# Kernel optimization log

Hardware: AMD Instinct MI355X
Metric: run time of the kernel (lower is better)

Reference implementation:

```python
import jax, jax.numpy as jnp
import numpy as np

N = 25000   # num nodes
E = 500000  # num edges
B = 4       # num queries (batch)
D = 32      # hidden dim
R2 = 474    # doubled num_relation
L = 4       # num conv layers
EPS = 1e-6


def setup_inputs() -> dict:
    key = jax.random.key(0)
    ks = jax.random.split(key, 12)
    return {
        "node_in": jax.random.randint(ks[0], (E,), 0, N),
        "node_out": jax.random.randint(ks[1], (E,), 0, N),
        "relation": jax.random.randint(ks[2], (E,), 0, R2),
        "edge_weight": jnp.ones((E,), jnp.float32),
        "h_index": jax.random.randint(ks[3], (B,), 0, N),
        "r_index": jax.random.randint(ks[4], (B,), 0, R2),
        "query_embed": jax.random.normal(ks[5], (R2, D), jnp.float32) * 0.1,
        "rel_W": jax.random.normal(ks[6], (L, D, R2 * D), jnp.float32) * 0.05,
        "rel_b": jnp.zeros((L, R2 * D), jnp.float32),
        "lin_W": jax.random.normal(ks[7], (L, 13 * D, D), jnp.float32) * 0.05,
        "lin_b": jnp.zeros((L, D), jnp.float32),
        "mlp_W1": jax.random.normal(ks[8], (2 * D, 2 * D), jnp.float32) * 0.05,
        "mlp_b1": jnp.zeros((2 * D,), jnp.float32),
        "mlp_W2": jax.random.normal(ks[9], (2 * D, 1), jnp.float32) * 0.05,
        "mlp_b2": jnp.zeros((1,), jnp.float32),
    }


def _nbfnet(node_in, node_out, relation, h_index, r_index,
            edge_weight, query_embed, rel_W, rel_b, lin_W, lin_b,
            mlp_W1, mlp_b1, mlp_W2, mlp_b2):
    query = query_embed[r_index]                                   # [B, D]
    # boundary condition: query embedding placed at the head node of each query
    boundary = jnp.zeros((N, B, D), query.dtype).at[h_index, jnp.arange(B)].set(query)
    # append one self-entry per node (boundary message), as in the torch code
    node_out_ext = jnp.concatenate([node_out, jnp.arange(N)])      # [E+N]
    w_ext = jnp.concatenate([edge_weight, jnp.ones((N,), edge_weight.dtype)])[:, None, None]
    cnt = jax.ops.segment_sum(jnp.ones((E + N,), query.dtype), node_out_ext, N)[:, None, None]
    deg = jax.ops.segment_sum(edge_weight, node_out, N) + 1.0      # degree_out + 1, [N]
    scale = jnp.log(deg)
    scale = scale / scale.mean()
    scales = jnp.stack([jnp.ones_like(scale), scale, 1.0 / jnp.clip(scale, 0.01)], -1)  # [N,3]

    hidden = boundary
    for l in range(L):
        # dependent relation embeddings: [R2, B, D]
        rel_in = (query @ rel_W[l] + rel_b[l]).reshape(B, R2, D).transpose(1, 0, 2)
        # distmult message + boundary self-message: [E+N, B, D]
        msg = jnp.concatenate([rel_in[relation] * hidden[node_in], boundary], 0)
        mw = msg * w_ext
        mean = jax.ops.segment_sum(mw, node_out_ext, N) / cnt
        sq_mean = jax.ops.segment_sum(msg * mw, node_out_ext, N) / cnt
        mx = jax.ops.segment_max(mw, node_out_ext, N)
        mn = jax.ops.segment_min(mw, node_out_ext, N)
        std = jnp.sqrt(jnp.clip(sq_mean - mean * mean, EPS))
        feat = jnp.stack([mean, mx, mn, std], -1).reshape(N, B, 4 * D)   # PNA stats
        update = (feat[..., None] * scales[:, None, None, :]).reshape(N, B, 12 * D)
        hidden = jax.nn.relu(jnp.concatenate([hidden, update], -1) @ lin_W[l] + lin_b[l])

    feat = jnp.concatenate([hidden, jnp.broadcast_to(query[None], (N, B, D))], -1)  # [N,B,2D]
    h1 = jax.nn.relu(feat @ mlp_W1 + mlp_b1)
    score = (h1 @ mlp_W2 + mlp_b2)[..., 0]                          # [N, B]
    return score.T                                                  # [B, N]


def reference(node_in, node_out, relation, edge_weight, h_index, r_index,
              query_embed, rel_W, rel_b, lin_W, lin_b,
              mlp_W1, mlp_b1, mlp_W2, mlp_b2):
    return _nbfnet(node_in, node_out, relation, h_index, r_index,
                   edge_weight, query_embed, rel_W, rel_b, lin_W, lin_b,
                   mlp_W1, mlp_b1, mlp_W2, mlp_b2)
```

## Files before the change

kernel.cpp:

```cpp
#include <hip/hip_runtime.h>
#include <hip/hip_fp16.h>

#define NN  25000
#define EE  500000
#define BB  4
#define DD  32
#define LL  4
#define R2C 474
#define BD  128
#define THD 416
#define EPSF 1e-6f
#define WMH 13312

typedef _Float16 half8 __attribute__((ext_vector_type(8)));
typedef _Float16 h2v   __attribute__((ext_vector_type(2)));
typedef float    f32x4 __attribute__((ext_vector_type(4)));
typedef float    f2v   __attribute__((ext_vector_type(2)));

__global__ __launch_bounds__(256) void pidx_kernel(const int4* __restrict__ no4,
                                                   int* __restrict__ cnt,
                                                   int4* __restrict__ pidx4) {
  int i = blockIdx.x * 256 + threadIdx.x;
  if (i >= EE / 4) return;
  int4 d = no4[i];
  int4 r;
  r.x = atomicAdd(&cnt[d.x], 1);
  r.y = atomicAdd(&cnt[d.y], 1);
  r.z = atomicAdd(&cnt[d.z], 1);
  r.w = atomicAdd(&cnt[d.w], 1);
  pidx4[i] = r;
}

__global__ __launch_bounds__(256) void prep_kernel(const int* __restrict__ cnt,
                                                   int* __restrict__ base,
                                                   int* __restrict__ gcnt) {
  int n = blockIdx.x * 256 + threadIdx.x;
  if (n >= NN) return;
  base[n] = atomicAdd(gcnt, (cnt[n] + 1) & ~1);
}

__global__ __launch_bounds__(256) void scatter_kernel(const int4* __restrict__ ni4,
                                                      const int4* __restrict__ no4,
                                                      const int4* __restrict__ rl4,
                                                      const float4* __restrict__ ew4,
                                                      const int* __restrict__ base,
                                                      const int4* __restrict__ pidx4,
                                                      int2* __restrict__ ep) {
  int i = blockIdx.x * 256 + threadIdx.x;
  if (i >= EE / 4) return;
  int4 ni = ni4[i], no = no4[i], rl = rl4[i], pi = pidx4[i];
  float4 w = ew4[i];
  h2v wa = {(_Float16)w.x, (_Float16)w.x};
  h2v wb = {(_Float16)w.y, (_Float16)w.y};
  h2v wc = {(_Float16)w.z, (_Float16)w.z};
  h2v wd = {(_Float16)w.w, (_Float16)w.w};
  ep[base[no.x] + pi.x] = make_int2(ni.x | (rl.x << 15), *(int*)&wa);
  ep[base[no.y] + pi.y] = make_int2(ni.y | (rl.y << 15), *(int*)&wb);
  ep[base[no.z] + pi.z] = make_int2(ni.z | (rl.z << 15), *(int*)&wc);
  ep[base[no.w] + pi.w] = make_int2(ni.w | (rl.w << 15), *(int*)&wd);
}

__global__ __launch_bounds__(256) void wdeg_kernel(const int* __restrict__ base,
                                                   const int* __restrict__ cnt,
                                                   const int2* __restrict__ ep,
                                                   float* __restrict__ lg,
                                                   float* __restrict__ logsum) {
  int n = blockIdx.x * 256 + threadIdx.x;
  float v = 0.f;
  if (n < NN) {
    int b = base[n], c = cnt[n];
    float s = 0.f;
    for (int p = b; p < b + c; ++p) {
      int wi = ep[p].y;
      h2v wh = *reinterpret_cast<h2v*>(&wi);
      s += (float)wh.x;
    }
    v = logf(s + 1.0f);
    lg[n] = v;
  }
  __shared__ float red[256];
  red[threadIdx.x] = v; __syncthreads();
  for (int o = 128; o > 0; o >>= 1) {
    if (threadIdx.x < o) red[threadIdx.x] += red[threadIdx.x + o];
    __syncthreads();
  }
  if (threadIdx.x == 0) atomicAdd(logsum, red[0]);
}

__global__ __launch_bounds__(256) void wmbuild_kernel(const float* __restrict__ linW,
                                                      const int* __restrict__ r_index,
                                                      const float* __restrict__ qemb,
                                                      float* __restrict__ query,
                                                      _Float16* __restrict__ Wm) {
  if (blockIdx.x == 0 && threadIdx.x < 128) {
    int t = threadIdx.x; int b = t >> 5, d = t & 31;
    query[t] = qemb[r_index[b] * DD + d];
  }
  int idx = blockIdx.x * 256 + threadIdx.x;
  if (idx >= LL * WMH) return;
  int l = idx / WMH, rest = idx % WMH;
  int t = rest >> 10;
  int nt = (rest >> 9) & 1;
  int L = (rest >> 3) & 63;
  int j = rest & 7;
  int k = t * 32 + (L >> 4) * 8 + j;
  int n = nt * 16 + (L & 15);
  int wrow;
  if (k < 32) wrow = k;
  else {
    int kk = k - 32;
    int slab = kk >> 7, s = (kk >> 5) & 3, dd = kk & 31;
    wrow = DD + (dd * 4 + s) * 3 + slab;
  }
  Wm[idx] = (_Float16)linW[(size_t)l * THD * DD + (size_t)wrow * DD + n];
}

__global__ __launch_bounds__(256) void relin_all_kernel(const float* __restrict__ query,
                                                        const float* __restrict__ relW,
                                                        const float* __restrict__ relB,
                                                        __half* __restrict__ relIn) {
  int o = blockIdx.x * 256 + threadIdx.x;
  if (o >= LL * R2C * BD) return;
  int l = o / (R2C * BD);
  int rest = o % (R2C * BD);
  int r = rest >> 7, b = (rest >> 5) & 3, d = rest & 31;
  int col = r * DD + d;
  const float* W = relW + (size_t)l * DD * R2C * DD;
  float acc = relB[(size_t)l * R2C * DD + col];
  #pragma unroll
  for (int k = 0; k < DD; ++k)
    acc = fmaf(query[b * DD + k], W[(size_t)k * (R2C * DD) + col], acc);
  relIn[o] = __float2half(acc);
}

__device__ __forceinline__ void mfma_epilogue(const _Float16* sh,
                                              const _Float16* hinh,
                                              __half* houth,
                                              const float* lg,
                                              const float* logsum,
                                              const _Float16* Wm,
                                              const float* bias,
                                              const float* query,
                                              const int* h_index,
                                              int nbase, int lane, bool hzero) {
  const int m = lane & 15;
  const int q = lane >> 4;
  const int nl = m >> 2;
  const int n = nbase + nl;
  const int b = m & 3;
  const float sc = lg[n] * ((float)NN / logsum[0]);
  const _Float16 one = (_Float16)1.f;
  const _Float16 s1h = (_Float16)sc;
  const _Float16 s2h = (_Float16)(1.0f / fmaxf(sc, 0.01f));
  const _Float16* ssrc = sh + nl * 512 + b * 32 + q * 8;

  f32x4 c0 = {0.f, 0.f, 0.f, 0.f};
  f32x4 c1 = {0.f, 0.f, 0.f, 0.f};
  half8 a;
  if (hzero) {
    a = (half8)(_Float16)0.f;
    if (n == h_index[b]) {
      const float* qp = query + b * 32 + q * 8;
      #pragma unroll
      for (int j = 0; j < 8; ++j) a[j] = (_Float16)qp[j];
    }
  } else {
    a = *(const half8*)(hinh + (unsigned)n * BD + b * 32 + q * 8);
  }
  #pragma unroll
  for (int t = 0; t < 13; ++t) {
    if (t > 0) {
      const int slab = (t - 1) >> 2, s = (t - 1) & 3;
      a = *(const half8*)(ssrc + s * 128);
      const _Float16 sch = (slab == 0) ? one : ((slab == 1) ? s1h : s2h);
      half8 sv = {sch, sch, sch, sch, sch, sch, sch, sch};
      a = a * sv;
    }
    half8 b0 = *(const half8*)(Wm + (unsigned)(t * 2 + 0) * 512 + lane * 8);
    half8 b1 = *(const half8*)(Wm + (unsigned)(t * 2 + 1) * 512 + lane * 8);
    c0 = __builtin_amdgcn_mfma_f32_16x16x32_f16(a, b0, c0, 0, 0, 0);
    c1 = __builtin_amdgcn_mfma_f32_16x16x32_f16(a, b1, c1, 0, 0, 0);
  }
  const int col = lane & 15;
  const float bj0 = bias[col], bj1 = bias[col + 16];
  #pragma unroll
  for (int i = 0; i < 4; ++i) {
    const int mr = q * 4 + i;
    __half* dst = houth + (unsigned)(nbase + (mr >> 2)) * BD + (mr & 3) * 32 + col;
    dst[0]  = __float2half(fmaxf(c0[i] + bj0, 0.f));
    dst[16] = __float2half(fmaxf(c1[i] + bj1, 0.f));
  }
}

__global__ __launch_bounds__(256) void layer1_fused_kernel(
    const h2v* __restrict__ rel2, const int2* __restrict__ ep,
    const int* __restrict__ base, const int* __restrict__ cnt,
    const int* __restrict__ h_index, const float* __restrict__ query,
    const float* __restrict__ lg, const float* __restrict__ logsum,
    const _Float16* __restrict__ Wm, const float* __restrict__ bias,
    __half* __restrict__ houth) {
  __shared__ __align__(16) h2v sh[4][256];
  const int lane = threadIdx.x & 63;
  const int wid  = threadIdx.x >> 6;
  const int nbase = blockIdx.x * 4;
  const int n = nbase + wid;
  const int b = lane >> 4;
  const int d0 = (lane & 15) * 2;
  const float q0 = query[b * 32 + d0], q1 = query[b * 32 + d0 + 1];
  const int hb = h_index[b];
  const int beg = __builtin_amdgcn_readfirstlane(base[n]);
  const int cnn = __builtin_amdgcn_readfirstlane(cnt[n]);
  const float mb0 = (n == hb) ? q0 : 0.f;
  const float mb1 = (n == hb) ? q1 : 0.f;
  float sa0 = mb0, qa0 = mb0 * mb0, mx0 = mb0, mn0 = mb0;
  float sa1 = mb1, qa1 = mb1 * mb1, mx1 = mb1, mn1 = mb1;
  int matched = 0;
  for (int p = beg; p < beg + cnn; ++p) {
    int2 e = ep[p];
    if ((e.x & 0x7fff) == hb) {
      h2v rv = rel2[(unsigned)((unsigned)e.x >> 15) * 64 + lane];
      int wi = e.y;
      h2v wh = *reinterpret_cast<h2v*>(&wi);
      float w = (float)wh.x;
      float m0 = (float)rv.x * q0, mw0 = m0 * w;
      float m1 = (float)rv.y * q1, mw1 = m1 * w;
      sa0 += mw0; qa0 = fmaf(m0, mw0, qa0); mx0 = fmaxf(mx0, mw0); mn0 = fminf(mn0, mw0);
      sa1 += mw1; qa1 = fmaf(m1, mw1, qa1); mx1 = fmaxf(mx1, mw1); mn1 = fminf(mn1, mw1);
      ++matched;
    }
  }
  if (matched < cnn) {
    mx0 = fmaxf(mx0, 0.f); mn0 = fminf(mn0, 0.f);
    mx1 = fmaxf(mx1, 0.f); mn1 = fminf(mn1, 0.f);
  }
  const float invc = 1.0f / (float)(cnn + 1);
  const float mean0 = sa0 * invc, mean1 = sa1 * invc;
  const float sd0 = sqrtf(fmaxf(qa0 * invc - mean0 * mean0, EPSF));
  const float sd1 = sqrtf(fmaxf(qa1 * invc - mean1 * mean1, EPSF));
  sh[wid][lane]       = (h2v){(_Float16)mean0, (_Float16)mean1};
  sh[wid][64 + lane]  = (h2v){(_Float16)mx0, (_Float16)mx1};
  sh[wid][128 + lane] = (h2v){(_Float16)mn0, (_Float16)mn1};
  sh[wid][192 + lane] = (h2v){(_Float16)sd0, (_Float16)sd1};
  __syncthreads();
  if (threadIdx.x >= 64) return;
  mfma_epilogue((const _Float16*)&sh[0][0], nullptr, houth, lg, logsum,
                Wm, bias, query, h_index, nbase, lane, true);
}

__global__ __launch_bounds__(256) void layer_fused_kernel(
    const h2v* __restrict__ hin2, const h2v* __restrict__ rel2,
    const int2* __restrict__ ep, const int* __restrict__ base,
    const int* __restrict__ cnt, const int* __restrict__ h_index,
    const float* __restrict__ query, const float* __restrict__ lg,
    const float* __restrict__ logsum, const _Float16* __restrict__ Wm,
    const float* __restrict__ bias, __half* __restrict__ houth) {
  __shared__ __align__(16) h2v sh[4][256];
  const int lane = threadIdx.x & 63;
  const int wid  = threadIdx.x >> 6;
  const int nbase = blockIdx.x * 4;
  const int n = nbase + wid;
  const int b = lane >> 4;
  const int d0 = (lane & 15) * 2;
  const float q0 = query[b * 32 + d0], q1 = query[b * 32 + d0 + 1];
  const int hb = h_index[b];
  const int beg = __builtin_amdgcn_readfirstlane(base[n]);
  const int cnn = __builtin_amdgcn_readfirstlane(cnt[n]);
  const float mb0 = (n == hb) ? q0 : 0.f;
  const float mb1 = (n == hb) ? q1 : 0.f;
  float sa0 = mb0, qa0 = mb0 * mb0;
  float sa1 = mb1, qa1 = mb1 * mb1;
  h2v mx2 = {(_Float16)mb0, (_Float16)mb1};
  h2v mn2 = mx2;

#define PROC(EwInt, Hv, Rv) {                                                \
    int _wi = (EwInt);                                                       \
    h2v _wh = *reinterpret_cast<h2v*>(&_wi);                                 \
    h2v _mh = (Hv) * (Rv);                                                   \
    h2v _mwh = _mh * _wh;                                                    \
    mx2 = __builtin_elementwise_max(mx2, _mwh);                              \
    mn2 = __builtin_elementwise_min(mn2, _mwh);                              \
    f2v _mf = __builtin_convertvector(_mh, f2v);                             \
    f2v _mwf = __builtin_convertvector(_mwh, f2v);                           \
    sa0 += _mwf.x; sa1 += _mwf.y;                                            \
    qa0 = fmaf(_mf.x, _mwf.x, qa0); qa1 = fmaf(_mf.y, _mwf.y, qa1); }
#define ROWS(Ex, Hd, Rd) {                                                   \
    Hd = hin2[(unsigned)((Ex) & 0x7fff) * 64 + lane];                        \
    Rd = rel2[(unsigned)((unsigned)(Ex) >> 15) * 64 + lane]; }

  int p = beg;
  int rem = cnn;
  const int nb = rem >> 3;
  if (nb > 0) {
    int2 E0, E1, E2, E3, E4, E5, E6, E7;
    h2v H0, H1, H2, H3, H4, H5, H6, H7;
    h2v R0, R1, R2, R3, R4, R5, R6, R7;
    E0 = ep[p];     E1 = ep[p + 1]; E2 = ep[p + 2]; E3 = ep[p + 3];
    E4 = ep[p + 4]; E5 = ep[p + 5]; E6 = ep[p + 6]; E7 = ep[p + 7];
    ROWS(E0.x, H0, R0); ROWS(E1.x, H1, R1); ROWS(E2.x, H2, R2); ROWS(E3.x, H3, R3);
    ROWS(E4.x, H4, R4); ROWS(E5.x, H5, R5); ROWS(E6.x, H6, R6); ROWS(E7.x, H7, R7);
    for (int it = 1; it < nb; ++it) {
      const int pn = p + 8;
      int2 F0 = ep[pn],     F1 = ep[pn + 1], F2 = ep[pn + 2], F3 = ep[pn + 3];
      int2 F4 = ep[pn + 4], F5 = ep[pn + 5], F6 = ep[pn + 6], F7 = ep[pn + 7];
      h2v G0, G1, G2, G3, G4, G5, G6, G7;
      h2v S0, S1, S2, S3, S4, S5, S6, S7;
      ROWS(F0.x, G0, S0); ROWS(F1.x, G1, S1); ROWS(F2.x, G2, S2); ROWS(F3.x, G3, S3);
      ROWS(F4.x, G4, S4); ROWS(F5.x, G5, S5); ROWS(F6.x, G6, S6); ROWS(F7.x, G7, S7);
      PROC(E0.y, H0, R0); PROC(E1.y, H1, R1); PROC(E2.y, H2, R2); PROC(E3.y, H3, R3);
      PROC(E4.y, H4, R4); PROC(E5.y, H5, R5); PROC(E6.y, H6, R6); PROC(E7.y, H7, R7);
      E0 = F0; E1 = F1; E2 = F2; E3 = F3; E4 = F4; E5 = F5; E6 = F6; E7 = F7;
      H0 = G0; H1 = G1; H2 = G2; H3 = G3; H4 = G4; H5 = G5; H6 = G6; H7 = G7;
      R0 = S0; R1 = S1; R2 = S2; R3 = S3; R4 = S4; R5 = S5; R6 = S6; R7 = S7;
      p = pn;
    }
    PROC(E0.y, H0, R0); PROC(E1.y, H1, R1); PROC(E2.y, H2, R2); PROC(E3.y, H3, R3);
    PROC(E4.y, H4, R4); PROC(E5.y, H5, R5); PROC(E6.y, H6, R6); PROC(E7.y, H7, R7);
    p += 8;
    rem -= nb << 3;
  }
  if (rem >= 4) {
    int2 E0 = ep[p], E1 = ep[p + 1], E2 = ep[p + 2], E3 = ep[p + 3];
    h2v H0, H1, H2, H3, R0, R1, R2, R3;
    ROWS(E0.x, H0, R0); ROWS(E1.x, H1, R1); ROWS(E2.x, H2, R2); ROWS(E3.x, H3, R3);
    PROC(E0.y, H0, R0); PROC(E1.y, H1, R1); PROC(E2.y, H2, R2); PROC(E3.y, H3, R3);
    p += 4; rem -= 4;
  }
  for (; rem > 0; --rem, ++p) {
    int2 e = ep[p];
    h2v hv, rv;
    ROWS(e.x, hv, rv);
    PROC(e.y, hv, rv);
  }
#undef ROWS
#undef PROC
  const float invc = 1.0f / (float)(cnn + 1);
  const float mean0 = sa0 * invc, mean1 = sa1 * invc;
  const float sd0 = sqrtf(fmaxf(qa0 * invc - mean0 * mean0, EPSF));
  const float sd1 = sqrtf(fmaxf(qa1 * invc - mean1 * mean1, EPSF));
  sh[wid][lane]       = (h2v){(_Float16)mean0, (_Float16)mean1};
  sh[wid][64 + lane]  = mx2;
  sh[wid][128 + lane] = mn2;
  sh[wid][192 + lane] = (h2v){(_Float16)sd0, (_Float16)sd1};
  __syncthreads();
  if (threadIdx.x >= 64) return;
  mfma_epilogue((const _Float16*)&sh[0][0], (const _Float16*)hin2, houth,
                lg, logsum, Wm, bias, query, h_index, nbase, lane, false);
}

__global__ __launch_bounds__(128) void mlp_kernel(const __half* __restrict__ hinh,
                                                  const float* __restrict__ query,
                                                  const float* __restrict__ W1,
                                                  const float* __restrict__ b1,
                                                  const float* __restrict__ W2,
                                                  const float* __restrict__ b2,
                                                  float* __restrict__ out) {
  __shared__ float f2[BB][2 * DD];
  const int t = threadIdx.x;
  const int b = t >> 5, d = t & 31;
  const float qv = query[t];
  const float w2a = W2[d], w2b = W2[DD + d];
  const float b1a = b1[d], b1b = b1[DD + d];
  const float b2v = b2[0];
  const int NPBM = 8;
  int n0 = blockIdx.x * NPBM, n1 = min(n0 + NPBM, NN);
  for (int n = n0; n < n1; ++n) {
    f2[b][d]      = __half2float(hinh[(unsigned)n * BD + t]);
    f2[b][DD + d] = qv;
    float a0 = b1a, a1 = b1b;
    #pragma unroll
    for (int i = 0; i < 2 * DD; ++i) {
      float v = f2[b][i];
      a0 = fmaf(v, W1[i * 2 * DD + d], a0);
      a1 = fmaf(v, W1[i * 2 * DD + DD + d], a1);
    }
    a0 = fmaxf(a0, 0.f); a1 = fmaxf(a1, 0.f);
    float part = a0 * w2a + a1 * w2b;
    #pragma unroll
    for (int off = 16; off > 0; off >>= 1) part += __shfl_down(part, off, 32);
    if (d == 0) out[b * NN + n] = part + b2v;
  }
}

extern "C" void kernel_launch(void* const* d_in, const int* in_sizes, int n_in,
                              void* d_out, int out_size, void* d_ws, size_t ws_size,
                              hipStream_t stream) {
  const int*   node_in  = (const int*)d_in[0];
  const int*   node_out = (const int*)d_in[1];
  const int*   relation = (const int*)d_in[2];
  const float* ew       = (const float*)d_in[3];
  const int*   h_index  = (const int*)d_in[4];
  const int*   r_index  = (const int*)d_in[5];
  const float* qemb     = (const float*)d_in[6];
  const float* relW     = (const float*)d_in[7];
  const float* relB     = (const float*)d_in[8];
  const float* linW     = (const float*)d_in[9];
  const float* linB     = (const float*)d_in[10];
  const float* W1       = (const float*)d_in[11];
  const float* b1       = (const float*)d_in[12];
  const float* W2       = (const float*)d_in[13];
  const float* b2       = (const float*)d_in[14];
  float* out = (float*)d_out;

  char* ws = (char*)d_ws;
  size_t off = 0;
  auto alloc = [&](size_t bytes) -> char* {
    char* p = ws + off;
    off += (bytes + 255) & ~(size_t)255;
    return p;
  };
  __half*   h0     = (__half*)  alloc((size_t)NN * BD * 2);
  __half*   h1     = (__half*)  alloc((size_t)NN * BD * 2);
  __half*   relIn  = (__half*)  alloc((size_t)LL * R2C * BD * 2);
  _Float16* Wm     = (_Float16*)alloc((size_t)LL * WMH * 2);
  int2*     ep     = (int2*)    alloc(((size_t)EE + NN) * 8);
  int*      pidx   = (int*)     alloc((size_t)EE * 4);
  int*      base   = (int*)     alloc((size_t)NN * 4);
  int*      cnti   = (int*)     alloc((size_t)NN * 4);
  float*    lg     = (float*)   alloc((size_t)NN * 4);
  float*    query  = (float*)   alloc((size_t)BD * 4);
  float*    stats  = (float*)   alloc(256);

  hipMemsetAsync(cnti, 0, (size_t)NN * 4, stream);
  hipMemsetAsync(stats, 0, 256, stream);

  float* logsum = stats;
  int*   gcnt   = (int*)stats + 1;

  pidx_kernel   <<<(EE / 4 + 255) / 256, 256, 0, stream>>>((const int4*)node_out,
                                                           cnti, (int4*)pidx);
  prep_kernel   <<<(NN + 255) / 256, 256, 0, stream>>>(cnti, base, gcnt);
  scatter_kernel<<<(EE / 4 + 255) / 256, 256, 0, stream>>>(
      (const int4*)node_in, (const int4*)node_out, (const int4*)relation,
      (const float4*)ew, base, (const int4*)pidx, ep);
  wdeg_kernel   <<<(NN + 255) / 256, 256, 0, stream>>>(base, cnti, ep, lg, logsum);
  wmbuild_kernel<<<(LL * WMH + 255) / 256, 256, 0, stream>>>(linW, r_index, qemb,
                                                             query, Wm);
  relin_all_kernel<<<(LL * R2C * BD + 255) / 256, 256, 0, stream>>>(query, relW, relB, relIn);

  __half* hin = h0; __half* hout = h1;
  for (int l = 0; l < LL; ++l) {
    if (l == 0) {
      layer1_fused_kernel<<<NN / 4, 256, 0, stream>>>(
          (const h2v*)relIn, ep, base, cnti, h_index, query, lg, logsum,
          Wm, linB, hout);
    } else {
      layer_fused_kernel<<<NN / 4, 256, 0, stream>>>(
          (const h2v*)hin, (const h2v*)relIn + (size_t)l * R2C * 64,
          ep, base, cnti, h_index, query, lg, logsum,
          Wm + (size_t)l * WMH, linB + (size_t)l * DD, hout);
    }
    __half* tmp = hin; hin = hout; hout = tmp;
  }
  mlp_kernel<<<(NN + 7) / 8, 128, 0, stream>>>(hin, query, W1, b1, W2, b2, out);
}
```

Measured before the change: 290.5 us.

## Group nodes by in-degree for balanced waves; merge constant-prep kernels

Builds a degree histogram, scans it, and produces a node permutation sorted by (clamped) in-degree, so each 4-wave block in the layer kernels processes nodes of similar degree and waves within a block finish together. Layer kernels and the MFMA epilogue now read node ids through this order array for both gathers and output writes. Separately, the relation-projection and weight-repack kernels are merged into one launch, with relIn reading query embeddings directly. The cost is an extra small scan kernel, extra atomics, and an indirection that scatters output writes non-contiguously.

```diff
diff --git a/kernel.cpp b/kernel.cpp
--- a/kernel.cpp
+++ b/kernel.cpp
@@ -11,6 +11,8 @@
 #define THD 416
 #define EPSF 1e-6f
 #define WMH 13312
+#define RLB ((LL * R2C * BD + 255) / 256)
+#define WMB ((LL * WMH + 255) / 256)
 
 typedef _Float16 half8 __attribute__((ext_vector_type(8)));
 typedef _Float16 h2v   __attribute__((ext_vector_type(2)));
@@ -33,10 +35,26 @@
 
 __global__ __launch_bounds__(256) void prep_kernel(const int* __restrict__ cnt,
                                                    int* __restrict__ base,
-                                                   int* __restrict__ gcnt) {
+                                                   int* __restrict__ gcnt,
+                                                   int* __restrict__ dh) {
   int n = blockIdx.x * 256 + threadIdx.x;
   if (n >= NN) return;
-  base[n] = atomicAdd(gcnt, (cnt[n] + 1) & ~1);
+  int c = cnt[n];
+  base[n] = atomicAdd(gcnt, (c + 1) & ~1);
+  atomicAdd(&dh[min(c, 63)], 1);
+}
+
+__global__ __launch_bounds__(64) void dscan_kernel(const int* __restrict__ dh,
+                                                   int* __restrict__ dbase) {
+  int t = threadIdx.x;
+  int v = dh[t];
+  int s = v;
+  #pragma unroll
+  for (int o = 1; o < 64; o <<= 1) {
+    int u = __shfl_up(s, o, 64);
+    if (t >= o) s += u;
+  }
+  dbase[t] = s - v;
 }
 
 __global__ __launch_bounds__(256) void scatter_kernel(const int4* __restrict__ ni4,
@@ -63,6 +81,9 @@
 __global__ __launch_bounds__(256) void wdeg_kernel(const int* __restrict__ base,
                                                    const int* __restrict__ cnt,
                                                    const int2* __restrict__ ep,
+                                                   const int* __restrict__ dbase,
+                                                   int* __restrict__ dfill,
+                                                   int* __restrict__ order,
                                                    float* __restrict__ lg,
                                                    float* __restrict__ logsum) {
   int n = blockIdx.x * 256 + threadIdx.x;
@@ -77,6 +98,9 @@
     }
     v = logf(s + 1.0f);
     lg[n] = v;
+    int bin = min(c, 63);
+    int pos = dbase[bin] + atomicAdd(&dfill[bin], 1);
+    order[pos] = n;
   }
   __shared__ float red[256];
   red[threadIdx.x] = v; __syncthreads();
@@ -87,16 +111,35 @@
   if (threadIdx.x == 0) atomicAdd(logsum, red[0]);
 }
 
-__global__ __launch_bounds__(256) void wmbuild_kernel(const float* __restrict__ linW,
-                                                      const int* __restrict__ r_index,
-                                                      const float* __restrict__ qemb,
-                                                      float* __restrict__ query,
-                                                      _Float16* __restrict__ Wm) {
-  if (blockIdx.x == 0 && threadIdx.x < 128) {
+__global__ __launch_bounds__(256) void const_kernel(const int* __restrict__ r_index,
+                                                    const float* __restrict__ qemb,
+                                                    const float* __restrict__ relW,
+                                                    const float* __restrict__ relB,
+                                                    const float* __restrict__ linW,
+                                                    float* __restrict__ query,
+                                                    __half* __restrict__ relIn,
+                                                    _Float16* __restrict__ Wm) {
+  if (blockIdx.x < RLB) {
+    int o = blockIdx.x * 256 + threadIdx.x;
+    if (o >= LL * R2C * BD) return;
+    int l = o / (R2C * BD);
+    int rest = o % (R2C * BD);
+    int r = rest >> 7, b = (rest >> 5) & 3, d = rest & 31;
+    int col = r * DD + d;
+    const float* W = relW + (size_t)l * DD * R2C * DD;
+    const float* q = qemb + (size_t)r_index[b] * DD;
+    float acc = relB[(size_t)l * R2C * DD + col];
+    #pragma unroll
+    for (int k = 0; k < DD; ++k)
+      acc = fmaf(q[k], W[(size_t)k * (R2C * DD) + col], acc);
+    relIn[o] = __float2half(acc);
+    return;
+  }
+  if (blockIdx.x == RLB && threadIdx.x < 128) {
     int t = threadIdx.x; int b = t >> 5, d = t & 31;
     query[t] = qemb[r_index[b] * DD + d];
   }
-  int idx = blockIdx.x * 256 + threadIdx.x;
+  int idx = (blockIdx.x - RLB) * 256 + threadIdx.x;
   if (idx >= LL * WMH) return;
   int l = idx / WMH, rest = idx % WMH;
   int t = rest >> 10;
@@ -115,24 +158,6 @@
   Wm[idx] = (_Float16)linW[(size_t)l * THD * DD + (size_t)wrow * DD + n];
 }
 
-__global__ __launch_bounds__(256) void relin_all_kernel(const float* __restrict__ query,
-                                                        const float* __restrict__ relW,
-                                                        const float* __restrict__ relB,
-                                                        __half* __restrict__ relIn) {
-  int o = blockIdx.x * 256 + threadIdx.x;
-  if (o >= LL * R2C * BD) return;
-  int l = o / (R2C * BD);
-  int rest = o % (R2C * BD);
-  int r = rest >> 7, b = (rest >> 5) & 3, d = rest & 31;
-  int col = r * DD + d;
-  const float* W = relW + (size_t)l * DD * R2C * DD;
-  float acc = relB[(size_t)l * R2C * DD + col];
-  #pragma unroll
-  for (int k = 0; k < DD; ++k)
-    acc = fmaf(query[b * DD + k], W[(size_t)k * (R2C * DD) + col], acc);
-  relIn[o] = __float2half(acc);
-}
-
 __device__ __forceinline__ void mfma_epilogue(const _Float16* sh,
                                               const _Float16* hinh,
                                               __half* houth,
@@ -142,11 +167,12 @@
                                               const float* bias,
                                               const float* query,
                                               const int* h_index,
+                                              const int* order,
                                               int nbase, int lane, bool hzero) {
   const int m = lane & 15;
   const int q = lane >> 4;
   const int nl = m >> 2;
-  const int n = nbase + nl;
+  const int n = order[nbase + nl];
   const int b = m & 3;
   const float sc = lg[n] * ((float)NN / logsum[0]);
   const _Float16 one = (_Float16)1.f;
@@ -186,7 +212,8 @@
   #pragma unroll
   for (int i = 0; i < 4; ++i) {
     const int mr = q * 4 + i;
-    __half* dst = houth + (unsigned)(nbase + (mr >> 2)) * BD + (mr & 3) * 32 + col;
+    const int nn = order[nbase + (mr >> 2)];
+    __half* dst = houth + (unsigned)nn * BD + (mr & 3) * 32 + col;
     dst[0]  = __float2half(fmaxf(c0[i] + bj0, 0.f));
     dst[16] = __float2half(fmaxf(c1[i] + bj1, 0.f));
   }
@@ -195,6 +222,7 @@
 __global__ __launch_bounds__(256) void layer1_fused_kernel(
     const h2v* __restrict__ rel2, const int2* __restrict__ ep,
     const int* __restrict__ base, const int* __restrict__ cnt,
+    const int* __restrict__ order,
     const int* __restrict__ h_index, const float* __restrict__ query,
     const float* __restrict__ lg, const float* __restrict__ logsum,
     const _Float16* __restrict__ Wm, const float* __restrict__ bias,
@@ -203,7 +231,7 @@
   const int lane = threadIdx.x & 63;
   const int wid  = threadIdx.x >> 6;
   const int nbase = blockIdx.x * 4;
-  const int n = nbase + wid;
+  const int n = __builtin_amdgcn_readfirstlane(order[nbase + wid]);
   const int b = lane >> 4;
   const int d0 = (lane & 15) * 2;
   const float q0 = query[b * 32 + d0], q1 = query[b * 32 + d0 + 1];
@@ -244,13 +272,14 @@
   __syncthreads();
   if (threadIdx.x >= 64) return;
   mfma_epilogue((const _Float16*)&sh[0][0], nullptr, houth, lg, logsum,
-                Wm, bias, query, h_index, nbase, lane, true);
+                Wm, bias, query, h_index, order, nbase, lane, true);
 }
 
 __global__ __launch_bounds__(256) void layer_fused_kernel(
     const h2v* __restrict__ hin2, const h2v* __restrict__ rel2,
     const int2* __restrict__ ep, const int* __restrict__ base,
-    const int* __restrict__ cnt, const int* __restrict__ h_index,
+    const int* __restrict__ cnt, const int* __restrict__ order,
+    const int* __restrict__ h_index,
     const float* __restrict__ query, const float* __restrict__ lg,
     const float* __restrict__ logsum, const _Float16* __restrict__ Wm,
     const float* __restrict__ bias, __half* __restrict__ houth) {
@@ -258,7 +287,7 @@
   const int lane = threadIdx.x & 63;
   const int wid  = threadIdx.x >> 6;
   const int nbase = blockIdx.x * 4;
-  const int n = nbase + wid;
+  const int n = __builtin_amdgcn_readfirstlane(order[nbase + wid]);
   const int b = lane >> 4;
   const int d0 = (lane & 15) * 2;
   const float q0 = query[b * 32 + d0], q1 = query[b * 32 + d0 + 1];
@@ -344,7 +373,7 @@
   __syncthreads();
   if (threadIdx.x >= 64) return;
   mfma_epilogue((const _Float16*)&sh[0][0], (const _Float16*)hin2, houth,
-                lg, logsum, Wm, bias, query, h_index, nbase, lane, false);
+                lg, logsum, Wm, bias, query, h_index, order, nbase, lane, false);
 }
 
 __global__ __launch_bounds__(128) void mlp_kernel(const __half* __restrict__ hinh,
@@ -416,37 +445,42 @@
   int*      pidx   = (int*)     alloc((size_t)EE * 4);
   int*      base   = (int*)     alloc((size_t)NN * 4);
   int*      cnti   = (int*)     alloc((size_t)NN * 4);
+  int*      order  = (int*)     alloc((size_t)NN * 4);
   float*    lg     = (float*)   alloc((size_t)NN * 4);
   float*    query  = (float*)   alloc((size_t)BD * 4);
-  float*    stats  = (float*)   alloc(256);
+  int*      ctl    = (int*)     alloc(1024);
 
   hipMemsetAsync(cnti, 0, (size_t)NN * 4, stream);
-  hipMemsetAsync(stats, 0, 256, stream);
-
-  float* logsum = stats;
-  int*   gcnt   = (int*)stats + 1;
+  hipMemsetAsync(ctl, 0, 1024, stream);
+
+  float* logsum = (float*)ctl;
+  int*   gcnt   = ctl + 1;
+  int*   dh     = ctl + 64;
+  int*   dfill  = ctl + 128;
+  int*   dbase  = ctl + 192;
 
   pidx_kernel   <<<(EE / 4 + 255) / 256, 256, 0, stream>>>((const int4*)node_out,
                                                            cnti, (int4*)pidx);
-  prep_kernel   <<<(NN + 255) / 256, 256, 0, stream>>>(cnti, base, gcnt);
+  prep_kernel   <<<(NN + 255) / 256, 256, 0, stream>>>(cnti, base, gcnt, dh);
+  dscan_kernel  <<<1, 64, 0, stream>>>(dh, dbase);
   scatter_kernel<<<(EE / 4 + 255) / 256, 256, 0, stream>>>(
       (const int4*)node_in, (const int4*)node_out, (const int4*)relation,
       (const float4*)ew, base, (const int4*)pidx, ep);
-  wdeg_kernel   <<<(NN + 255) / 256, 256, 0, stream>>>(base, cnti, ep, lg, logsum);
-  wmbuild_kernel<<<(LL * WMH + 255) / 256, 256, 0, stream>>>(linW, r_index, qemb,
-                                                             query, Wm);
-  relin_all_kernel<<<(LL * R2C * BD + 255) / 256, 256, 0, stream>>>(query, relW, relB, relIn);
+  wdeg_kernel   <<<(NN + 255) / 256, 256, 0, stream>>>(base, cnti, ep, dbase,
+                                                       dfill, order, lg, logsum);
+  const_kernel  <<<RLB + WMB, 256, 0, stream>>>(r_index, qemb, relW, relB, linW,
+                                                query, relIn, Wm);
 
   __half* hin = h0; __half* hout = h1;
   for (int l = 0; l < LL; ++l) {
     if (l == 0) {
       layer1_fused_kernel<<<NN / 4, 256, 0, stream>>>(
-          (const h2v*)relIn, ep, base, cnti, h_index, query, lg, logsum,
+          (const h2v*)relIn, ep, base, cnti, order, h_index, query, lg, logsum,
           Wm, linB, hout);
     } else {
       layer_fused_kernel<<<NN / 4, 256, 0, stream>>>(
           (const h2v*)hin, (const h2v*)relIn + (size_t)l * R2C * 64,
-          ep, base, cnti, h_index, query, lg, logsum,
+          ep, base, cnti, order, h_index, query, lg, logsum,
           Wm + (size_t)l * WMH, linB + (size_t)l * DD, hout);
     }
     __half* tmp = hin; hin = hout; hout = tmp;
```

New measurement: 423.5 us. 45.8% more time.
